# Performance work log

Measured on AMD Instinct MI355X. Metric: run time of the kernel, lower is better.

The kernel has to match this reference:

```python
import jax, jax.numpy as jnp
import numpy as np

Q, C, SHOT, D = 8192, 64, 5, 512


def setup_inputs() -> dict:
    key = jax.random.key(0)
    kx, ky = jax.random.split(key)
    x = jax.random.normal(kx, (Q, D), dtype=jnp.float32)
    y = jax.random.normal(ky, (C, SHOT, D), dtype=jnp.float32)
    return {"x": x, "y": y}


def reference(x, y):
    # x: [q, d] queries (already flat). y: [C, shot, d] support sets.
    q = x.reshape(x.shape[0], -1)                      # [q, d]
    proto = y.reshape(y.shape[0], y.shape[1], -1).mean(axis=1)  # [C, d]
    # broadcasted L1 distance: [q, C]
    dist = jnp.abs(q[:, None, :] - proto[None, :, :]).sum(axis=-1)
    return jax.nn.softmax(-dist, axis=1)
```

## Files before the change

kernel.cpp:

```cpp
#include <hip/hip_runtime.h>
#include <hip/hip_bf16.h>
#include <math.h>

#define QN 8192
#define CN 64
#define SHOT 5
#define DN 512

#define THREADS 256
#define WAVES 4
#define TQ 4
#define QPB (WAVES * TQ)
#define DCHUNK 256
#define F4 (DCHUNK / 4)
#define LDS_F4 (CN * F4)

__global__ void proto_kernel(const float* __restrict__ y, float* __restrict__ proto) {
    int idx = blockIdx.x * blockDim.x + threadIdx.x;
    if (idx < CN * DN) {
        int c = idx >> 9;
        int d = idx & (DN - 1);
        float s = 0.f;
#pragma unroll
        for (int sh = 0; sh < SHOT; ++sh)
            s += y[(c * SHOT + sh) * DN + d];
        proto[idx] = s * (1.0f / SHOT);
    }
}

__global__ __launch_bounds__(THREADS, 2) void dist_softmax_kernel(
        const float* __restrict__ x,
        const float* __restrict__ proto,
        float* __restrict__ out) {
    __shared__ float4 plds[LDS_F4];

    const int tid  = threadIdx.x;
    const int lane = tid & 63;
    const int wave = __builtin_amdgcn_readfirstlane(tid >> 6);
    const int q0   = blockIdx.x * QPB + wave * TQ;

    const float4* proto4 = (const float4*)proto;

    float acc[TQ];
#pragma unroll
    for (int i = 0; i < TQ; ++i) acc[i] = 0.f;

    for (int d0 = 0; d0 < DN; d0 += DCHUNK) {
        const int f0 = d0 >> 2;
#pragma unroll
        for (int k = 0; k < LDS_F4 / THREADS; ++k) {
            int i = tid + k * THREADS;
            int c = i >> 6;
            int f = i & (F4 - 1);
            plds[c * F4 + (f ^ (c & 7))] = proto4[c * (DN / 4) + f0 + f];
        }
        __syncthreads();

        const float* xb = x + q0 * DN + d0;
#pragma unroll 4
        for (int f = 0; f < F4; ++f) {
            float4 p = plds[lane * F4 + (f ^ (lane & 7))];
#pragma unroll
            for (int qi = 0; qi < TQ; ++qi) {
                float4 a = *(const float4*)(xb + qi * DN + f * 4);
                acc[qi] += fabsf(a.x - p.x) + fabsf(a.y - p.y)
                         + fabsf(a.z - p.z) + fabsf(a.w - p.w);
            }
        }
        __syncthreads();
    }

#pragma unroll
    for (int qi = 0; qi < TQ; ++qi) {
        float nd = -acc[qi];
        float m = nd;
#pragma unroll
        for (int off = 32; off; off >>= 1)
            m = fmaxf(m, __shfl_xor(m, off, 64));
        float e = __expf(nd - m);
        float s = e;
#pragma unroll
        for (int off = 32; off; off >>= 1)
            s += __shfl_xor(s, off, 64);
        out[(q0 + qi) * CN + lane] = e / s;
    }
}

extern "C" void kernel_launch(void* const* d_in, const int* in_sizes, int n_in,
                              void* d_out, int out_size, void* d_ws, size_t ws_size,
                              hipStream_t stream) {
    const float* x = (const float*)d_in[0];
    const float* y = (const float*)d_in[1];
    float* out     = (float*)d_out;
    float* proto   = (float*)d_ws;

    proto_kernel<<<(CN * DN + 255) / 256, 256, 0, stream>>>(y, proto);
    dist_softmax_kernel<<<QN / QPB, THREADS, 0, stream>>>(x, proto, out);
}
```

Before: 36.54 us.

## Double-buffer proto and x chunks into LDS via async global_load_lds

Result: slower. 41.51 us (+13.6%).

```diff
diff --git a/kernel.cpp b/kernel.cpp
--- a/kernel.cpp
+++ b/kernel.cpp
@@ -8,14 +8,15 @@
 #define DN 512
 
 #define THREADS 256
-#define WAVES 4
+#define NWAVES 4
 #define TQ 4
-#define QPB (WAVES * TQ)
-#define DCHUNK 256
-#define F4 (DCHUNK / 4)
-#define LDS_F4 (CN * F4)
+#define QPB (NWAVES * TQ)
+#define DCHUNK 128
+#define F4C (DCHUNK / 4)
+#define NCHUNK (DN / DCHUNK)
+#define DMA_PER_WAVE 10
 
-__global__ void proto_kernel(const float* __restrict__ y, float* __restrict__ proto) {
+__global__ void proto_kernel(const float* __restrict__ y, float* __restrict__ pws) {
     int idx = blockIdx.x * blockDim.x + threadIdx.x;
     if (idx < CN * DN) {
         int c = idx >> 9;
@@ -24,55 +25,82 @@
 #pragma unroll
         for (int sh = 0; sh < SHOT; ++sh)
             s += y[(c * SHOT + sh) * DN + d];
-        proto[idx] = s * (1.0f / SHOT);
+        int g   = d >> 2;
+        int sub = d & 3;
+        int gs  = (g & ~31) | ((g & 31) ^ (c & 7));
+        pws[c * DN + gs * 4 + sub] = s * (1.0f / SHOT);
     }
 }
 
 __global__ __launch_bounds__(THREADS, 2) void dist_softmax_kernel(
         const float* __restrict__ x,
-        const float* __restrict__ proto,
+        const float* __restrict__ pws,
         float* __restrict__ out) {
-    __shared__ float4 plds[LDS_F4];
+    __shared__ float4 pbuf[2][CN * F4C];
+    __shared__ float4 xbuf[2][QPB * F4C];
 
     const int tid  = threadIdx.x;
     const int lane = tid & 63;
     const int wave = __builtin_amdgcn_readfirstlane(tid >> 6);
-    const int q0   = blockIdx.x * QPB + wave * TQ;
+    const int q0b  = blockIdx.x * QPB;
+    const int lhi  = lane >> 5;
+    const int llo  = lane & 31;
 
-    const float4* proto4 = (const float4*)proto;
+    auto issue = [&](int k) {
+        const int buf = k & 1;
+#pragma unroll
+        for (int t = 0; t < 8; ++t) {
+            int i = wave * 8 + t;
+            const float* src = pws + (((2 * i + lhi) * (DN / 4) + k * F4C + llo) << 2);
+            __builtin_amdgcn_global_load_lds(
+                (const __attribute__((address_space(1))) void*)src,
+                (__attribute__((address_space(3))) void*)&pbuf[buf][i * 64], 16, 0, 0);
+        }
+#pragma unroll
+        for (int t = 0; t < 2; ++t) {
+            int j = wave * 2 + t;
+            const float* src = x + (((q0b + 2 * j + lhi) * (DN / 4) + k * F4C + llo) << 2);
+            __builtin_amdgcn_global_load_lds(
+                (const __attribute__((address_space(1))) void*)src,
+                (__attribute__((address_space(3))) void*)&xbuf[buf][j * 64], 16, 0, 0);
+        }
+    };
 
-    float acc[TQ];
-#pragma unroll
-    for (int i = 0; i < TQ; ++i) acc[i] = 0.f;
+    float acc0 = 0.f, acc1 = 0.f, acc2 = 0.f, acc3 = 0.f;
 
-    for (int d0 = 0; d0 < DN; d0 += DCHUNK) {
-        const int f0 = d0 >> 2;
-#pragma unroll
-        for (int k = 0; k < LDS_F4 / THREADS; ++k) {
-            int i = tid + k * THREADS;
-            int c = i >> 6;
-            int f = i & (F4 - 1);
-            plds[c * F4 + (f ^ (c & 7))] = proto4[c * (DN / 4) + f0 + f];
+    issue(0);
+    for (int k = 0; k < NCHUNK; ++k) {
+        if (k < NCHUNK - 1) {
+            issue(k + 1);
+            asm volatile("s_waitcnt vmcnt(10)" ::: "memory");
+        } else {
+            asm volatile("s_waitcnt vmcnt(0)" ::: "memory");
         }
-        __syncthreads();
+        __builtin_amdgcn_s_barrier();
+        __builtin_amdgcn_sched_barrier(0);
 
-        const float* xb = x + q0 * DN + d0;
-#pragma unroll 4
-        for (int f = 0; f < F4; ++f) {
-            float4 p = plds[lane * F4 + (f ^ (lane & 7))];
-#pragma unroll
-            for (int qi = 0; qi < TQ; ++qi) {
-                float4 a = *(const float4*)(xb + qi * DN + f * 4);
-                acc[qi] += fabsf(a.x - p.x) + fabsf(a.y - p.y)
-                         + fabsf(a.z - p.z) + fabsf(a.w - p.w);
-            }
+        const float4* pB = pbuf[k & 1] + lane * F4C;
+        const float4* xB = xbuf[k & 1] + (wave * TQ) * F4C;
+        const int ls7 = lane & 7;
+#pragma unroll 8
+        for (int f = 0; f < F4C; ++f) {
+            float4 p  = pB[f ^ ls7];
+            float4 a0 = xB[f];
+            float4 a1 = xB[F4C + f];
+            float4 a2 = xB[2 * F4C + f];
+            float4 a3 = xB[3 * F4C + f];
+            acc0 += fabsf(a0.x - p.x) + fabsf(a0.y - p.y) + fabsf(a0.z - p.z) + fabsf(a0.w - p.w);
+            acc1 += fabsf(a1.x - p.x) + fabsf(a1.y - p.y) + fabsf(a1.z - p.z) + fabsf(a1.w - p.w);
+            acc2 += fabsf(a2.x - p.x) + fabsf(a2.y - p.y) + fabsf(a2.z - p.z) + fabsf(a2.w - p.w);
+            acc3 += fabsf(a3.x - p.x) + fabsf(a3.y - p.y) + fabsf(a3.z - p.z) + fabsf(a3.w - p.w);
         }
-        __syncthreads();
+        __builtin_amdgcn_s_barrier();
     }
 
+    float accs[TQ] = {acc0, acc1, acc2, acc3};
 #pragma unroll
     for (int qi = 0; qi < TQ; ++qi) {
-        float nd = -acc[qi];
+        float nd = -accs[qi];
         float m = nd;
 #pragma unroll
         for (int off = 32; off; off >>= 1)
@@ -82,7 +110,7 @@
 #pragma unroll
         for (int off = 32; off; off >>= 1)
             s += __shfl_xor(s, off, 64);
-        out[(q0 + qi) * CN + lane] = e / s;
+        out[(q0b + wave * TQ + qi) * CN + lane] = e / s;
     }
 }
 
@@ -92,8 +120,8 @@
     const float* x = (const float*)d_in[0];
     const float* y = (const float*)d_in[1];
     float* out     = (float*)d_out;
-    float* proto   = (float*)d_ws;
+    float* pws     = (float*)d_ws;
 
-    proto_kernel<<<(CN * DN + 255) / 256, 256, 0, stream>>>(y, proto);
-    dist_softmax_kernel<<<QN / QPB, THREADS, 0, stream>>>(x, proto, out);
+    proto_kernel<<<(CN * DN + 255) / 256, 256, 0, stream>>>(y, pws);
+    dist_softmax_kernel<<<QN / QPB, THREADS, 0, stream>>>(x, pws, out);
 }
```

## Split D across blocks with partial sums and separate softmax kernel

Applied to the files above, without the earlier changes.

Result: faster. 31.24 us (-14.5%).

```diff
diff --git a/kernel.cpp b/kernel.cpp
--- a/kernel.cpp
+++ b/kernel.cpp
@@ -7,13 +7,13 @@
 #define SHOT 5
 #define DN 512
 
+#define SPLIT 4
+#define DSLICE (DN / SPLIT)
+#define F4S (DSLICE / 4)
 #define THREADS 256
-#define WAVES 4
-#define TQ 4
-#define QPB (WAVES * TQ)
-#define DCHUNK 256
-#define F4 (DCHUNK / 4)
-#define LDS_F4 (CN * F4)
+#define NWAVES 4
+#define TQ 8
+#define QPB (NWAVES * TQ)
 
 __global__ void proto_kernel(const float* __restrict__ y, float* __restrict__ proto) {
     int idx = blockIdx.x * blockDim.x + threadIdx.x;
@@ -28,62 +28,78 @@
     }
 }
 
-__global__ __launch_bounds__(THREADS, 2) void dist_softmax_kernel(
+__global__ __launch_bounds__(THREADS, 4) void dist_kernel(
         const float* __restrict__ x,
         const float* __restrict__ proto,
-        float* __restrict__ out) {
-    __shared__ float4 plds[LDS_F4];
+        float* __restrict__ partial) {
+    __shared__ float4 plds[CN * F4S];
 
-    const int tid  = threadIdx.x;
-    const int lane = tid & 63;
-    const int wave = __builtin_amdgcn_readfirstlane(tid >> 6);
-    const int q0   = blockIdx.x * QPB + wave * TQ;
+    const int tid   = threadIdx.x;
+    const int lane  = tid & 63;
+    const int wave  = __builtin_amdgcn_readfirstlane(tid >> 6);
+    const int split = blockIdx.x & (SPLIT - 1);
+    const int qb    = blockIdx.x >> 2;
+    const int d0    = split * DSLICE;
+    const int q0    = qb * QPB + wave * TQ;
 
     const float4* proto4 = (const float4*)proto;
+#pragma unroll
+    for (int k = 0; k < (CN * F4S) / THREADS; ++k) {
+        int i = tid + k * THREADS;
+        int c = i >> 5;
+        int f = i & 31;
+        plds[c * F4S + (f ^ (c & 7))] = proto4[c * (DN / 4) + (d0 >> 2) + f];
+    }
+    __syncthreads();
 
     float acc[TQ];
 #pragma unroll
     for (int i = 0; i < TQ; ++i) acc[i] = 0.f;
 
-    for (int d0 = 0; d0 < DN; d0 += DCHUNK) {
-        const int f0 = d0 >> 2;
+    const float4* xb = (const float4*)(x + (size_t)q0 * DN + d0);
+    const float4* pB = plds + lane * F4S;
+    const int ls = lane & 7;
+
 #pragma unroll
-        for (int k = 0; k < LDS_F4 / THREADS; ++k) {
-            int i = tid + k * THREADS;
-            int c = i >> 6;
-            int f = i & (F4 - 1);
-            plds[c * F4 + (f ^ (c & 7))] = proto4[c * (DN / 4) + f0 + f];
+    for (int f = 0; f < F4S; ++f) {
+        float4 p = pB[f ^ ls];
+#pragma unroll
+        for (int qi = 0; qi < TQ; ++qi) {
+            float4 a = xb[qi * (DN / 4) + f];
+            acc[qi] += fabsf(a.x - p.x) + fabsf(a.y - p.y)
+                     + fabsf(a.z - p.z) + fabsf(a.w - p.w);
         }
-        __syncthreads();
-
-        const float* xb = x + q0 * DN + d0;
-#pragma unroll 4
-        for (int f = 0; f < F4; ++f) {
-            float4 p = plds[lane * F4 + (f ^ (lane & 7))];
-#pragma unroll
-            for (int qi = 0; qi < TQ; ++qi) {
-                float4 a = *(const float4*)(xb + qi * DN + f * 4);
-                acc[qi] += fabsf(a.x - p.x) + fabsf(a.y - p.y)
-                         + fabsf(a.z - p.z) + fabsf(a.w - p.w);
-            }
-        }
-        __syncthreads();
     }
 
 #pragma unroll
-    for (int qi = 0; qi < TQ; ++qi) {
-        float nd = -acc[qi];
-        float m = nd;
+    for (int qi = 0; qi < TQ; ++qi)
+        partial[((size_t)split * QN + q0 + qi) * CN + lane] = acc[qi];
+}
+
+__global__ __launch_bounds__(THREADS, 4) void softmax_kernel(
+        const float* __restrict__ partial,
+        float* __restrict__ out) {
+    const int tid  = threadIdx.x;
+    const int lane = tid & 63;
+    const int wave = tid >> 6;
+    const int q    = blockIdx.x * NWAVES + wave;
+
+    float s = 0.f;
 #pragma unroll
-        for (int off = 32; off; off >>= 1)
-            m = fmaxf(m, __shfl_xor(m, off, 64));
-        float e = __expf(nd - m);
-        float s = e;
+    for (int sp = 0; sp < SPLIT; ++sp)
+        s += partial[((size_t)sp * QN + q) * CN + lane];
+
+    float nd = -s;
+    float m = nd;
 #pragma unroll
-        for (int off = 32; off; off >>= 1)
-            s += __shfl_xor(s, off, 64);
-        out[(q0 + qi) * CN + lane] = e / s;
-    }
+    for (int off = 32; off; off >>= 1)
+        m = fmaxf(m, __shfl_xor(m, off, 64));
+    float e = __expf(nd - m);
+    float t = e;
+#pragma unroll
+    for (int off = 32; off; off >>= 1)
+        t += __shfl_xor(t, off, 64);
+    out[(size_t)q * CN + lane] = e / t;
 }
 
 extern "C" void kernel_launch(void* const* d_in, const int* in_sizes, int n_in,
@@ -93,7 +109,9 @@
     const float* y = (const float*)d_in[1];
     float* out     = (float*)d_out;
     float* proto   = (float*)d_ws;
+    float* partial = (float*)d_ws + (size_t)CN * DN;
 
     proto_kernel<<<(CN * DN + 255) / 256, 256, 0, stream>>>(y, proto);
-    dist_softmax_kernel<<<QN / QPB, THREADS, 0, stream>>>(x, proto, out);
+    dist_kernel<<<(QN / QPB) * SPLIT, THREADS, 0, stream>>>(x, proto, partial);
+    softmax_kernel<<<QN / NWAVES, THREADS, 0, stream>>>(partial, out);
 }
```
